# Optimization experiments

Measured on AMD Instinct MI355X. Metric: run time of the kernel, lower is better.

The kernel has to match this reference:

```python
import jax, jax.numpy as jnp
import numpy as np

B, H, W, C = 32, 64, 64, 256
NH, WS, SS = 8, 8, 4
N = WS * WS
HD = C // NH
MLP_HID = 4 * C


def _rel_pos_index(ws):
    coords = np.stack(np.meshgrid(np.arange(ws), np.arange(ws), indexing='ij'))  # [2,ws,ws]
    cf = coords.reshape(2, -1)                      # [2,N]
    rc = (cf[:, :, None] - cf[:, None, :]).transpose(1, 2, 0)  # [N,N,2]
    rc[..., 0] += ws - 1
    rc[..., 1] += ws - 1
    rc[..., 0] *= 2 * ws - 1
    return rc.sum(-1)                               # [N,N] int


def _attn_mask(h, w, ws, ss):
    # Swin shifted-window mask: -100 where tokens come from different regions
    img = np.zeros((h, w))
    cnt = 0
    for hs in (slice(0, -ws), slice(-ws, -ss), slice(-ss, None)):
        for wsl in (slice(0, -ws), slice(-ws, -ss), slice(-ss, None)):
            img[hs, wsl] = cnt
            cnt += 1
    mw = img.reshape(h // ws, ws, w // ws, ws).transpose(0, 2, 1, 3).reshape(-1, ws * ws)  # [nW,N]
    diff = mw[:, None, :] - mw[:, :, None]
    return np.where(diff != 0, -100.0, 0.0).astype(np.float32)  # [nW,N,N]


_RPI = jnp.asarray(_rel_pos_index(WS))          # [N,N]
_MASK = jnp.asarray(_attn_mask(H, W, WS, SS))   # [nW,N,N]


def _ln(x, w, b, eps=1e-5):
    mu = x.mean(-1, keepdims=True)
    var = ((x - mu) ** 2).mean(-1, keepdims=True)
    return (x - mu) * jax.lax.rsqrt(var + eps) * w + b


def setup_inputs() -> dict:
    key = jax.random.key(0)
    ks = jax.random.split(key, 6)
    s = 0.02
    return {
        'x': jax.random.normal(ks[0], (B, H * W, C), jnp.float32),
        'norm1_w': jnp.ones((C,), jnp.float32),
        'norm1_b': jnp.zeros((C,), jnp.float32),
        'qkv_w': jax.random.normal(ks[1], (3 * C, C), jnp.float32) * s,
        'qkv_b': jnp.zeros((3 * C,), jnp.float32),
        'rpb_table': jax.random.normal(ks[2], ((2 * WS - 1) ** 2, NH), jnp.float32) * s,
        'proj_w': jax.random.normal(ks[3], (C, C), jnp.float32) * s,
        'proj_b': jnp.zeros((C,), jnp.float32),
        'norm2_w': jnp.ones((C,), jnp.float32),
        'norm2_b': jnp.zeros((C,), jnp.float32),
        'fc1_w': jax.random.normal(ks[4], (MLP_HID, C), jnp.float32) * s,
        'fc1_b': jnp.zeros((MLP_HID,), jnp.float32),
        'fc2_w': jax.random.normal(ks[5], (C, MLP_HID), jnp.float32) * s,
        'fc2_b': jnp.zeros((C,), jnp.float32),
    }


def reference(x, norm1_w, norm1_b, qkv_w, qkv_b, rpb_table, proj_w, proj_b,
              norm2_w, norm2_b, fc1_w, fc1_b, fc2_w, fc2_b):
    scale = HD ** -0.5
    nW = (H // WS) * (W // WS)

    shortcut = x
    h = _ln(x, norm1_w, norm1_b).reshape(B, H, W, C)
    # cyclic shift
    h = jnp.roll(h, shift=(-SS, -SS), axis=(1, 2))
    # window partition -> [B*nW, N, C]
    xw = h.reshape(B, H // WS, WS, W // WS, WS, C).transpose(0, 1, 3, 2, 4, 5).reshape(-1, N, C)

    qkv = xw @ qkv_w.T + qkv_b                      # [B*nW, N, 3C]
    qkv = qkv.reshape(-1, N, 3, NH, HD).transpose(2, 0, 3, 1, 4)  # [3, B*nW, NH, N, HD]
    q, k, v = qkv[0] * scale, qkv[1], qkv[2]

    attn = jnp.einsum('bhnd,bhmd->bhnm', q, k)      # [B*nW, NH, N, N]
    bias = rpb_table[_RPI.reshape(-1)].reshape(N, N, NH).transpose(2, 0, 1)  # [NH,N,N]
    attn = attn + bias[None]
    attn = (attn.reshape(B, nW, NH, N, N) + _MASK[None, :, None]).reshape(-1, NH, N, N)
    attn = jax.nn.softmax(attn, axis=-1)

    out = jnp.einsum('bhnm,bhmd->bhnd', attn, v)    # [B*nW, NH, N, HD]
    out = out.transpose(0, 2, 1, 3).reshape(-1, N, C)
    out = out @ proj_w.T + proj_b

    # window reverse + reverse shift
    out = out.reshape(B, H // WS, W // WS, WS, WS, C).transpose(0, 1, 3, 2, 4, 5).reshape(B, H, W, C)
    out = jnp.roll(out, shift=(SS, SS), axis=(1, 2)).reshape(B, H * W, C)

    x1 = shortcut + out
    h2 = _ln(x1, norm2_w, norm2_b)
    h2 = jax.nn.gelu(h2 @ fc1_w.T + fc1_b, approximate=False)
    h2 = h2 @ fc2_w.T + fc2_b
    return x1 + h2
```

## Files before the change

kernel.cpp:

```cpp
#include <hip/hip_runtime.h>
#include <hip/hip_bf16.h>

#define DEVI __device__ __forceinline__

using f32x4  = __attribute__((ext_vector_type(4))) float;
using bf16x8 = __attribute__((ext_vector_type(8))) short;
using s16x4  = __attribute__((ext_vector_type(4))) short;

DEVI float b2f(unsigned short u) {
  unsigned int x = ((unsigned int)u) << 16;
  return __uint_as_float(x);
}
DEVI unsigned short f2b(float f) {
  unsigned int x = __float_as_uint(f);
  unsigned int r = x + 0x7fffu + ((x >> 16) & 1u);
  return (unsigned short)(r >> 16);
}

DEVI void gload_lds16(const void* g, void* l) {
  __builtin_amdgcn_global_load_lds(
      (const __attribute__((address_space(1))) void*)g,
      (__attribute__((address_space(3))) void*)l, 16, 0, 0);
}

constexpr int kB = 32, kH = 64, kW = 64, kC = 256;
constexpr int kNH = 8, kWS = 8, kSS = 4, kN = 64, kHD = 32;
constexpr int kTOK = kB * kH * kW;
constexpr int kMLP = 4 * kC;

__global__ void conv_bf16(const float* __restrict__ src,
                          unsigned short* __restrict__ dst, int n4) {
  int i = blockIdx.x * blockDim.x + threadIdx.x;
  if (i < n4) {
    float4 v = *reinterpret_cast<const float4*>(src + (size_t)i * 4);
    s16x4 o;
    o[0] = (short)f2b(v.x); o[1] = (short)f2b(v.y);
    o[2] = (short)f2b(v.z); o[3] = (short)f2b(v.w);
    *reinterpret_cast<s16x4*>(dst + (size_t)i * 4) = o;
  }
}

__global__ __launch_bounds__(256) void ln1_shift_win(
    const float* __restrict__ x, const float* __restrict__ w,
    const float* __restrict__ bb, unsigned short* __restrict__ xw) {
  int wave = threadIdx.x >> 6, lane = threadIdx.x & 63;
  int t_dst = blockIdx.x * 4 + wave;
  int widx = t_dst >> 6, tok = t_dst & 63;
  int b = widx >> 6, win = widx & 63;
  int wh = win >> 3, ww = win & 7;
  int y = tok >> 3, xx = tok & 7;
  int r = (wh * 8 + y + kSS) & 63;
  int c = (ww * 8 + xx + kSS) & 63;
  const float* src = x + ((size_t)b * 4096 + r * 64 + c) * kC;

  float4 v = *reinterpret_cast<const float4*>(src + lane * 4);
  float s  = v.x + v.y + v.z + v.w;
  float s2 = v.x * v.x + v.y * v.y + v.z * v.z + v.w * v.w;
#pragma unroll
  for (int o = 32; o > 0; o >>= 1) {
    s  += __shfl_xor(s, o);
    s2 += __shfl_xor(s2, o);
  }
  float mu = s * (1.f / kC);
  float var = s2 * (1.f / kC) - mu * mu;
  float rstd = rsqrtf(var + 1e-5f);
  float4 wv = *reinterpret_cast<const float4*>(w + lane * 4);
  float4 bv = *reinterpret_cast<const float4*>(bb + lane * 4);
  s16x4 o;
  o[0] = (short)f2b((v.x - mu) * rstd * wv.x + bv.x);
  o[1] = (short)f2b((v.y - mu) * rstd * wv.y + bv.y);
  o[2] = (short)f2b((v.z - mu) * rstd * wv.z + bv.z);
  o[3] = (short)f2b((v.w - mu) * rstd * wv.w + bv.w);
  *reinterpret_cast<s16x4*>(xw + (size_t)t_dst * kC + lane * 4) = o;
}

template <int EPI, typename OUT_T>
__global__ __launch_bounds__(256) void gemm_bt(
    const unsigned short* __restrict__ A, const unsigned short* __restrict__ Bw,
    const float* __restrict__ bias, OUT_T* __restrict__ Co,
    const float* __restrict__ res, int M, int Nc, int K) {
  constexpr int BM = 128, BN = 128, BK = 64;
  __shared__ unsigned short sA[BM * BK];
  __shared__ unsigned short sB[BN * BK];
  int tid = threadIdx.x;
  int lane = tid & 63, wave = tid >> 6;
  int nbn = Nc / BN;
  int bm = (blockIdx.x / nbn) * BM;
  int bn = (blockIdx.x % nbn) * BN;
  int wr = wave >> 1, wc = wave & 1;

  f32x4 acc[4][4];
#pragma unroll
  for (int m = 0; m < 4; ++m)
#pragma unroll
    for (int n = 0; n < 4; ++n) acc[m][n] = (f32x4){0.f, 0.f, 0.f, 0.f};

  for (int k0 = 0; k0 < K; k0 += BK) {
#pragma unroll
    for (int it = 0; it < 4; ++it) {
      int c = it * 256 + tid;
      int row = c >> 3;
      int kc = (c & 7) * 8;
      const unsigned short* gA = A + (size_t)(bm + row) * K + k0 + kc;
      const unsigned short* gB = Bw + (size_t)(bn + row) * K + k0 + kc;
      char* lA = (char*)sA + (it * 256 + wave * 64) * 16;
      char* lB = (char*)sB + (it * 256 + wave * 64) * 16;
      gload_lds16(gA, lA);
      gload_lds16(gB, lB);
    }
    __syncthreads();
#pragma unroll
    for (int kk = 0; kk < 2; ++kk) {
      bf16x8 af[4], bfr[4];
#pragma unroll
      for (int m = 0; m < 4; ++m) {
        int row = wr * 64 + m * 16 + (lane & 15);
        af[m] = *reinterpret_cast<const bf16x8*>(
            &sA[row * BK + kk * 32 + (lane >> 4) * 8]);
      }
#pragma unroll
      for (int n = 0; n < 4; ++n) {
        int row = wc * 64 + n * 16 + (lane & 15);
        bfr[n] = *reinterpret_cast<const bf16x8*>(
            &sB[row * BK + kk * 32 + (lane >> 4) * 8]);
      }
#pragma unroll
      for (int m = 0; m < 4; ++m)
#pragma unroll
        for (int n = 0; n < 4; ++n)
          acc[m][n] = __builtin_amdgcn_mfma_f32_16x16x32_bf16(
              af[m], bfr[n], acc[m][n], 0, 0, 0);
    }
    __syncthreads();
  }

#pragma unroll
  for (int m = 0; m < 4; ++m) {
#pragma unroll
    for (int n = 0; n < 4; ++n) {
      int row0 = bm + wr * 64 + m * 16 + ((lane >> 4) << 2);
      int col = bn + wc * 64 + n * 16 + (lane & 15);
      float bcol = bias[col];
#pragma unroll
      for (int i = 0; i < 4; ++i) {
        float v = acc[m][n][i] + bcol;
        size_t idx = (size_t)(row0 + i) * Nc + col;
        if constexpr (EPI == 1) {
          v = 0.5f * v * (1.0f + erff(v * 0.70710678118654752f));
        }
        if constexpr (EPI == 2) {
          v += res[idx];
        }
        if constexpr (sizeof(OUT_T) == 2) {
          Co[idx] = (OUT_T)f2b(v);
        } else {
          Co[idx] = v;
        }
      }
    }
  }
}

__global__ __launch_bounds__(64) void attn_win(
    const unsigned short* __restrict__ qkv, const float* __restrict__ rpb,
    unsigned short* __restrict__ outb) {
  __shared__ float kf[64][33];
  __shared__ float vf[64][33];
  int t = threadIdx.x;
  int widx = blockIdx.x >> 3, h = blockIdx.x & 7;
  int win = widx & 63;
  int wh = win >> 3, ww = win & 7;
  size_t base = ((size_t)widx * 64 + t) * 768;

  const unsigned short* kp = qkv + base + 256 + h * 32;
  const unsigned short* vp = qkv + base + 512 + h * 32;
#pragma unroll
  for (int i = 0; i < 8; ++i) {
    s16x4 k4 = *reinterpret_cast<const s16x4*>(kp + i * 4);
    s16x4 v4 = *reinterpret_cast<const s16x4*>(vp + i * 4);
#pragma unroll
    for (int j = 0; j < 4; ++j) {
      kf[t][i * 4 + j] = b2f((unsigned short)k4[j]);
      vf[t][i * 4 + j] = b2f((unsigned short)v4[j]);
    }
  }
  float q[32];
  const unsigned short* qp = qkv + base + h * 32;
  constexpr float scale = 0.17677669529663687f;
#pragma unroll
  for (int i = 0; i < 8; ++i) {
    s16x4 q4 = *reinterpret_cast<const s16x4*>(qp + i * 4);
#pragma unroll
    for (int j = 0; j < 4; ++j) q[i * 4 + j] = b2f((unsigned short)q4[j]) * scale;
  }
  __syncthreads();

  int yi = t >> 3, xi = t & 7;
  int gyi = wh * 8 + yi, gxi = ww * 8 + xi;
  int ryi = gyi < 56 ? 0 : (gyi < 60 ? 1 : 2);
  int rxi = gxi < 56 ? 0 : (gxi < 60 ? 1 : 2);

  float m = -1e30f, l = 0.f;
  float acc[32];
#pragma unroll
  for (int d = 0; d < 32; ++d) acc[d] = 0.f;

  for (int j = 0; j < 64; ++j) {
    int yj = j >> 3, xj = j & 7;
    float s = rpb[((yi - yj + 7) * 15 + (xi - xj + 7)) * 8 + h];
    int gyj = wh * 8 + yj, gxj = ww * 8 + xj;
    int ryj = gyj < 56 ? 0 : (gyj < 60 ? 1 : 2);
    int rxj = gxj < 56 ? 0 : (gxj < 60 ? 1 : 2);
    if ((ryi != ryj) || (rxi != rxj)) s -= 100.f;
#pragma unroll
    for (int d = 0; d < 32; ++d) s += q[d] * kf[j][d];
    float mn = fmaxf(m, s);
    float sc = __expf(m - mn);
    float p = __expf(s - mn);
    l = l * sc + p;
#pragma unroll
    for (int d = 0; d < 32; ++d) acc[d] = acc[d] * sc + p * vf[j][d];
    m = mn;
  }
  float rl = 1.f / l;
  unsigned short* op = outb + ((size_t)widx * 64 + t) * 256 + h * 32;
#pragma unroll
  for (int i = 0; i < 8; ++i) {
    s16x4 o;
#pragma unroll
    for (int j = 0; j < 4; ++j) o[j] = (short)f2b(acc[i * 4 + j] * rl);
    *reinterpret_cast<s16x4*>(op + i * 4) = o;
  }
}

__global__ __launch_bounds__(256) void resid_ln2(
    const float* __restrict__ x, const unsigned short* __restrict__ proj,
    const float* __restrict__ w2, const float* __restrict__ b2,
    float* __restrict__ x1out, unsigned short* __restrict__ ln2out) {
  int wave = threadIdx.x >> 6, lane = threadIdx.x & 63;
  int t = blockIdx.x * 4 + wave;
  int b = t >> 12, p = t & 4095;
  int r = p >> 6, c = p & 63;
  int rr = (r + 64 - kSS) & 63;
  int cc = (c + 64 - kSS) & 63;
  int widx = b * 64 + (rr >> 3) * 8 + (cc >> 3);
  int tok = (rr & 7) * 8 + (cc & 7);
  size_t srow = ((size_t)widx * 64 + tok) * 256;

  float4 xv = *reinterpret_cast<const float4*>(x + (size_t)t * kC + lane * 4);
  s16x4 pv = *reinterpret_cast<const s16x4*>(proj + srow + lane * 4);
  float v0 = xv.x + b2f((unsigned short)pv[0]);
  float v1 = xv.y + b2f((unsigned short)pv[1]);
  float v2 = xv.z + b2f((unsigned short)pv[2]);
  float v3 = xv.w + b2f((unsigned short)pv[3]);

  float4 o4; o4.x = v0; o4.y = v1; o4.z = v2; o4.w = v3;
  *reinterpret_cast<float4*>(x1out + (size_t)t * kC + lane * 4) = o4;

  float s = v0 + v1 + v2 + v3;
  float s2 = v0 * v0 + v1 * v1 + v2 * v2 + v3 * v3;
#pragma unroll
  for (int o = 32; o > 0; o >>= 1) {
    s  += __shfl_xor(s, o);
    s2 += __shfl_xor(s2, o);
  }
  float mu = s * (1.f / kC);
  float var = s2 * (1.f / kC) - mu * mu;
  float rstd = rsqrtf(var + 1e-5f);
  float4 wv = *reinterpret_cast<const float4*>(w2 + lane * 4);
  float4 bv = *reinterpret_cast<const float4*>(b2 + lane * 4);
  s16x4 o;
  o[0] = (short)f2b((v0 - mu) * rstd * wv.x + bv.x);
  o[1] = (short)f2b((v1 - mu) * rstd * wv.y + bv.y);
  o[2] = (short)f2b((v2 - mu) * rstd * wv.z + bv.z);
  o[3] = (short)f2b((v3 - mu) * rstd * wv.w + bv.w);
  *reinterpret_cast<s16x4*>(ln2out + (size_t)t * kC + lane * 4) = o;
}

extern "C" void kernel_launch(void* const* d_in, const int* in_sizes, int n_in,
                              void* d_out, int out_size, void* d_ws,
                              size_t ws_size, hipStream_t stream) {
  const float* x      = (const float*)d_in[0];
  const float* n1w    = (const float*)d_in[1];
  const float* n1b    = (const float*)d_in[2];
  const float* qkvw   = (const float*)d_in[3];
  const float* qkvb   = (const float*)d_in[4];
  const float* rpb    = (const float*)d_in[5];
  const float* projw  = (const float*)d_in[6];
  const float* projb  = (const float*)d_in[7];
  const float* n2w    = (const float*)d_in[8];
  const float* n2b    = (const float*)d_in[9];
  const float* fc1w   = (const float*)d_in[10];
  const float* fc1b   = (const float*)d_in[11];
  const float* fc2w   = (const float*)d_in[12];
  const float* fc2b   = (const float*)d_in[13];
  float* out = (float*)d_out;

  unsigned short* wq = (unsigned short*)d_ws;
  unsigned short* wp = wq + 768 * 256;
  unsigned short* w1 = wp + 256 * 256;
  unsigned short* w2 = w1 + 1024 * 256;
  unsigned short* bufA = w2 + 256 * 1024;
  unsigned short* bufB = bufA + (size_t)kTOK * kC;

  conv_bf16<<<192, 256, 0, stream>>>(qkvw, wq, 49152);
  conv_bf16<<<64, 256, 0, stream>>>(projw, wp, 16384);
  conv_bf16<<<256, 256, 0, stream>>>(fc1w, w1, 65536);
  conv_bf16<<<256, 256, 0, stream>>>(fc2w, w2, 65536);

  ln1_shift_win<<<kTOK / 4, 256, 0, stream>>>(x, n1w, n1b, bufA);

  gemm_bt<0, unsigned short><<<(kTOK / 128) * (768 / 128), 256, 0, stream>>>(
      bufA, wq, qkvb, bufB, nullptr, kTOK, 768, kC);

  attn_win<<<(kTOK / 64) * kNH, 64, 0, stream>>>(bufB, rpb, bufA);

  gemm_bt<0, unsigned short><<<(kTOK / 128) * (kC / 128), 256, 0, stream>>>(
      bufA, wp, projb, bufB, nullptr, kTOK, kC, kC);

  resid_ln2<<<kTOK / 4, 256, 0, stream>>>(x, bufB, n2w, n2b, out, bufA);

  gemm_bt<1, unsigned short><<<(kTOK / 128) * (kMLP / 128), 256, 0, stream>>>(
      bufA, w1, fc1b, bufB, nullptr, kTOK, kMLP, kC);

  gemm_bt<2, float><<<(kTOK / 128) * (kC / 128), 256, 0, stream>>>(
      bufB, w2, fc2b, out, out, kTOK, kC, kMLP);
}
```

Measured before the change: 1.155 ms.

## Rewrite windowed attention with bf16 MFMA for QK^T and PV

Replaces the per-token scalar online-softmax attention kernel with one that gives each wave a full window and loops over heads. QK^T and PV run on 16x16x32 bf16 MFMA instructions. The softmax is done in registers with cross-lane shuffles, and P and transposed V are staged in LDS. This removes the scalar FMA-bound inner loop, at the cost of rounding P to bf16 and relying on per-wave LDS use without explicit barriers.

Result: faster. 990.7 us (-14.2%).

```diff
diff --git a/kernel.cpp b/kernel.cpp
--- a/kernel.cpp
+++ b/kernel.cpp
@@ -161,75 +161,141 @@
   }
 }
 
-__global__ __launch_bounds__(64) void attn_win(
+__global__ __launch_bounds__(128) void attn_mfma(
     const unsigned short* __restrict__ qkv, const float* __restrict__ rpb,
     unsigned short* __restrict__ outb) {
-  __shared__ float kf[64][33];
-  __shared__ float vf[64][33];
-  int t = threadIdx.x;
-  int widx = blockIdx.x >> 3, h = blockIdx.x & 7;
+  constexpr int PS = 72;
+  __shared__ unsigned short lds[2][(64 + 32) * PS];
+  int lane = threadIdx.x & 63, wave = threadIdx.x >> 6;
+  int widx = blockIdx.x * 2 + wave;
   int win = widx & 63;
   int wh = win >> 3, ww = win & 7;
-  size_t base = ((size_t)widx * 64 + t) * 768;
-
-  const unsigned short* kp = qkv + base + 256 + h * 32;
-  const unsigned short* vp = qkv + base + 512 + h * 32;
-#pragma unroll
-  for (int i = 0; i < 8; ++i) {
-    s16x4 k4 = *reinterpret_cast<const s16x4*>(kp + i * 4);
-    s16x4 v4 = *reinterpret_cast<const s16x4*>(vp + i * 4);
-#pragma unroll
-    for (int j = 0; j < 4; ++j) {
-      kf[t][i * 4 + j] = b2f((unsigned short)k4[j]);
-      vf[t][i * 4 + j] = b2f((unsigned short)v4[j]);
-    }
-  }
-  float q[32];
-  const unsigned short* qp = qkv + base + h * 32;
+  unsigned short* P  = lds[wave];
+  unsigned short* VT = lds[wave] + 64 * PS;
+  int l15 = lane & 15, g = lane >> 4;
+  int gh = g >> 1;
+  size_t wbase = (size_t)widx * 64 * 768;
   constexpr float scale = 0.17677669529663687f;
-#pragma unroll
-  for (int i = 0; i < 8; ++i) {
-    s16x4 q4 = *reinterpret_cast<const s16x4*>(qp + i * 4);
-#pragma unroll
-    for (int j = 0; j < 4; ++j) q[i * 4 + j] = b2f((unsigned short)q4[j]) * scale;
-  }
-  __syncthreads();
-
-  int yi = t >> 3, xi = t & 7;
-  int gyi = wh * 8 + yi, gxi = ww * 8 + xi;
-  int ryi = gyi < 56 ? 0 : (gyi < 60 ? 1 : 2);
-  int rxi = gxi < 56 ? 0 : (gxi < 60 ? 1 : 2);
-
-  float m = -1e30f, l = 0.f;
-  float acc[32];
-#pragma unroll
-  for (int d = 0; d < 32; ++d) acc[d] = 0.f;
-
-  for (int j = 0; j < 64; ++j) {
-    int yj = j >> 3, xj = j & 7;
-    float s = rpb[((yi - yj + 7) * 15 + (xi - xj + 7)) * 8 + h];
-    int gyj = wh * 8 + yj, gxj = ww * 8 + xj;
-    int ryj = gyj < 56 ? 0 : (gyj < 60 ? 1 : 2);
-    int rxj = gxj < 56 ? 0 : (gxj < 60 ? 1 : 2);
-    if ((ryi != ryj) || (rxi != rxj)) s -= 100.f;
-#pragma unroll
-    for (int d = 0; d < 32; ++d) s += q[d] * kf[j][d];
-    float mn = fmaxf(m, s);
-    float sc = __expf(m - mn);
-    float p = __expf(s - mn);
-    l = l * sc + p;
-#pragma unroll
-    for (int d = 0; d < 32; ++d) acc[d] = acc[d] * sc + p * vf[j][d];
-    m = mn;
-  }
-  float rl = 1.f / l;
-  unsigned short* op = outb + ((size_t)widx * 64 + t) * 256 + h * 32;
-#pragma unroll
-  for (int i = 0; i < 8; ++i) {
-    s16x4 o;
-#pragma unroll
-    for (int j = 0; j < 4; ++j) o[j] = (short)f2b(acc[i * 4 + j] * rl);
-    *reinterpret_cast<s16x4*>(op + i * 4) = o;
+
+  int xj = l15 & 7;
+  int gxj = ww * 8 + xj;
+  int rxj = gxj < 56 ? 0 : (gxj < 60 ? 1 : 2);
+  int yj_[4], ryj_[4];
+#pragma unroll
+  for (int n = 0; n < 4; ++n) {
+    yj_[n] = 2 * n + (l15 >> 3);
+    int gyj = wh * 8 + yj_[n];
+    ryj_[n] = gyj < 56 ? 0 : (gyj < 60 ? 1 : 2);
+  }
+  int rxok_[4], dx8_[4];
+#pragma unroll
+  for (int i = 0; i < 4; ++i) {
+    int xi = (g & 1) * 4 + i;
+    int gxi = ww * 8 + xi;
+    int rxi = gxi < 56 ? 0 : (gxi < 60 ? 1 : 2);
+    rxok_[i] = (rxi == rxj);
+    dx8_[i] = (xi - xj + 7) * 8;
+  }
+
+  for (int h = 0; h < 8; ++h) {
+    const unsigned short* qb = qkv + wbase + h * 32;
+    bf16x8 qf[4], kf[4];
+#pragma unroll
+    for (int m = 0; m < 4; ++m)
+      qf[m] = *reinterpret_cast<const bf16x8*>(qb + (size_t)(16 * m + l15) * 768 + g * 8);
+#pragma unroll
+    for (int n = 0; n < 4; ++n)
+      kf[n] = *reinterpret_cast<const bf16x8*>(qb + 256 + (size_t)(16 * n + l15) * 768 + g * 8);
+
+    f32x4 S[4][4];
+#pragma unroll
+    for (int m = 0; m < 4; ++m)
+#pragma unroll
+      for (int n = 0; n < 4; ++n) S[m][n] = (f32x4){0.f, 0.f, 0.f, 0.f};
+#pragma unroll
+    for (int m = 0; m < 4; ++m)
+#pragma unroll
+      for (int n = 0; n < 4; ++n)
+        S[m][n] = __builtin_amdgcn_mfma_f32_16x16x32_bf16(qf[m], kf[n], S[m][n], 0, 0, 0);
+
+    bf16x8 vrow[4];
+#pragma unroll
+    for (int i2 = 0; i2 < 4; ++i2)
+      vrow[i2] = *reinterpret_cast<const bf16x8*>(qb + 512 + (size_t)lane * 768 + i2 * 8);
+#pragma unroll
+    for (int i2 = 0; i2 < 4; ++i2)
+#pragma unroll
+      for (int j = 0; j < 8; ++j)
+        VT[(i2 * 8 + j) * PS + lane] = (unsigned short)vrow[i2][j];
+
+#pragma unroll
+    for (int m = 0; m < 4; ++m) {
+      int yi = 2 * m + gh;
+      int gyi = wh * 8 + yi;
+      int ryi = gyi < 56 ? 0 : (gyi < 60 ? 1 : 2);
+      int dy120_[4], rok_[4];
+#pragma unroll
+      for (int n = 0; n < 4; ++n) {
+        dy120_[n] = (yi - yj_[n] + 7) * 120;
+        rok_[n] = (ryi == ryj_[n]);
+      }
+#pragma unroll
+      for (int i = 0; i < 4; ++i) {
+        float t[4];
+#pragma unroll
+        for (int n = 0; n < 4; ++n) {
+          float bias = rpb[dy120_[n] + dx8_[i] + h];
+          float msk = (rok_[n] && rxok_[i]) ? 0.f : -100.f;
+          t[n] = fmaf(S[m][n][i], scale, bias + msk);
+        }
+        float mx = fmaxf(fmaxf(t[0], t[1]), fmaxf(t[2], t[3]));
+#pragma unroll
+        for (int o = 1; o < 16; o <<= 1) mx = fmaxf(mx, __shfl_xor(mx, o));
+        float sm = 0.f;
+#pragma unroll
+        for (int n = 0; n < 4; ++n) {
+          t[n] = __expf(t[n] - mx);
+          sm += t[n];
+        }
+#pragma unroll
+        for (int o = 1; o < 16; o <<= 1) sm += __shfl_xor(sm, o);
+        float rl = 1.f / sm;
+        int rowoff = (16 * m + 4 * g + i) * PS;
+#pragma unroll
+        for (int n = 0; n < 4; ++n)
+          P[rowoff + 16 * n + l15] = f2b(t[n] * rl);
+      }
+    }
+
+    f32x4 O[4][2];
+#pragma unroll
+    for (int m = 0; m < 4; ++m)
+#pragma unroll
+      for (int n2 = 0; n2 < 2; ++n2) O[m][n2] = (f32x4){0.f, 0.f, 0.f, 0.f};
+#pragma unroll
+    for (int kk = 0; kk < 2; ++kk) {
+      bf16x8 pa[4], vb[2];
+#pragma unroll
+      for (int m = 0; m < 4; ++m)
+        pa[m] = *reinterpret_cast<const bf16x8*>(&P[(16 * m + l15) * PS + kk * 32 + g * 8]);
+#pragma unroll
+      for (int n2 = 0; n2 < 2; ++n2)
+        vb[n2] = *reinterpret_cast<const bf16x8*>(&VT[(16 * n2 + l15) * PS + kk * 32 + g * 8]);
+#pragma unroll
+      for (int m = 0; m < 4; ++m)
+#pragma unroll
+        for (int n2 = 0; n2 < 2; ++n2)
+          O[m][n2] = __builtin_amdgcn_mfma_f32_16x16x32_bf16(pa[m], vb[n2], O[m][n2], 0, 0, 0);
+    }
+
+    unsigned short* ob = outb + (size_t)widx * 64 * 256 + h * 32;
+#pragma unroll
+    for (int m = 0; m < 4; ++m)
+#pragma unroll
+      for (int n2 = 0; n2 < 2; ++n2)
+#pragma unroll
+        for (int i = 0; i < 4; ++i)
+          ob[(16 * m + 4 * g + i) * 256 + 16 * n2 + l15] = f2b(O[m][n2][i]);
   }
 }
 
@@ -313,7 +379,7 @@
   gemm_bt<0, unsigned short><<<(kTOK / 128) * (768 / 128), 256, 0, stream>>>(
       bufA, wq, qkvb, bufB, nullptr, kTOK, 768, kC);
 
-  attn_win<<<(kTOK / 64) * kNH, 64, 0, stream>>>(bufB, rpb, bufA);
+  attn_mfma<<<(kTOK / 64) / 2, 128, 0, stream>>>(bufB, rpb, bufA);
 
   gemm_bt<0, unsigned short><<<(kTOK / 128) * (kC / 128), 256, 0, stream>>>(
       bufA, wp, projb, bufB, nullptr, kTOK, kC, kC);
```
